# Kernel optimization log

Hardware: AMD Instinct MI355X
Metric: run time of the kernel (lower is better)

The kernel has to match this reference:

```python
import jax, jax.numpy as jnp
import numpy as np

N, DQ, T, H1 = 131072, 256, 4, 512

def setup_inputs() -> dict:
    key = jax.random.key(0)
    k_q, k_w0, k_b0, k_w1, k_z = jax.random.split(key, 5)
    return {
        "q": jax.random.normal(k_q, (N, DQ), dtype=jnp.float32),
        "Z": jax.random.randint(k_z, (N,), 0, T, dtype=jnp.int32),
        "W0": jax.random.normal(k_w0, (T, DQ, H1), dtype=jnp.float32) * (1.0 / np.sqrt(DQ)),
        "b0": jax.random.normal(k_b0, (T, H1), dtype=jnp.float32) * 0.01,
        "W1": jax.random.normal(k_w1, (T, H1), dtype=jnp.float32) * (1.0 / np.sqrt(H1)),
        "b1": jnp.zeros((), dtype=jnp.float32),
    }

def reference(q, Z, W0, b0, W1, b1):
    # Dense grouped-GEMM over all T types (T is small), then select per-atom
    # type result. Avoids materializing the per-atom [N, dq, h1] gathered
    # weight tensor that tf.gather would create.
    h_all = jnp.einsum('nd,tdh->nth', q, W0)              # [N, T, H1]
    h = jnp.take_along_axis(h_all, Z[:, None, None].astype(jnp.int32), axis=1)[:, 0, :]  # [N, H1]
    h = jnp.tanh(h + b0[Z])                               # hidden activations
    F = jnp.einsum('nh,nh->n', h, W1[Z]) + b1             # [N]
    return F
```

## Files before the change

### kernel.cpp

```cpp
#include <hip/hip_runtime.h>
#include <hip/hip_bf16.h>

#define N_ATOMS 131072
#define DQ 256
#define H1 512
#define NTYPES 4
#define TILE_M 64
#define NPAD (N_ATOMS + NTYPES * TILE_M)
#define BLOCKS_PER_TYPE 64

typedef __bf16 bf16x8 __attribute__((ext_vector_type(8)));
typedef float f32x16 __attribute__((ext_vector_type(16)));

__device__ __forceinline__ unsigned short f2bf(float f) {
  unsigned int u = __builtin_bit_cast(unsigned int, f);
  u += 0x7fffu + ((u >> 16) & 1u);
  return (unsigned short)(u >> 16);
}
__device__ __forceinline__ unsigned int pack2(float a, float b) {
  return (unsigned int)f2bf(a) | ((unsigned int)f2bf(b) << 16);
}
__device__ __forceinline__ float fast_tanh(float x) {
  float e = __expf(2.0f * x);
  return 1.0f - 2.0f * __builtin_amdgcn_rcpf(e + 1.0f);
}

__global__ __launch_bounds__(256) void hist_kernel(
    const int* __restrict__ Z, int* __restrict__ perm,
    int* __restrict__ blockcounts)
{
  const int b = blockIdx.x, tid = threadIdx.x;
  const int gid = b * 256 + tid;
  for (int i = gid; i < NPAD; i += 512 * 256) perm[i] = -1;
  __shared__ int lc[NTYPES];
  if (tid < NTYPES) lc[tid] = 0;
  __syncthreads();
  atomicAdd(&lc[Z[gid]], 1);
  __syncthreads();
  if (tid < NTYPES) blockcounts[b * NTYPES + tid] = lc[tid];
}

__global__ __launch_bounds__(256) void w0s_kernel(
    const float* __restrict__ W0, unsigned short* __restrict__ W0s)
{
  __shared__ __align__(16) unsigned short S[64][72];
  const int b = blockIdx.x;
  const int nb = b & 7, kb = (b >> 3) & 3, t = b >> 5;
  const int tid = threadIdx.x;
  const int kl = tid >> 4, nl = (tid & 15) * 4;
#pragma unroll
  for (int r = 0; r < 4; ++r) {
    const int k = r * 16 + kl;
    const float4 v = *(const float4*)&W0[((size_t)(t * DQ + kb * 64 + k)) * H1 + nb * 64 + nl];
    S[nl + 0][k] = f2bf(v.x);
    S[nl + 1][k] = f2bf(v.y);
    S[nl + 2][k] = f2bf(v.z);
    S[nl + 3][k] = f2bf(v.w);
  }
  __syncthreads();
#pragma unroll
  for (int r = 0; r < 2; ++r) {
    const int c = r * 256 + tid;
    const int n = c & 63, kg2l = c >> 6;
    const uint4 v = *(const uint4*)&S[n][kg2l * 8];
    ((uint4*)W0s)[(size_t)(t * 32 + kb * 8 + kg2l) * H1 + nb * 64 + n] = v;
  }
}

__global__ __launch_bounds__(256) void scan_kernel(
    const int* __restrict__ blockcounts, int* __restrict__ padded_off,
    int* __restrict__ cursors)
{
  __shared__ int sums[NTYPES];
  const int tid = threadIdx.x;
  if (tid < NTYPES) sums[tid] = 0;
  __syncthreads();
  const int t = tid & 3;
  int acc = 0;
  for (int b = tid >> 2; b < 512; b += 64) acc += blockcounts[b * 4 + t];
  atomicAdd(&sums[t], acc);
  __syncthreads();
  if (tid == 0) {
    int off = 0;
#pragma unroll
    for (int i = 0; i < NTYPES; ++i) {
      padded_off[i] = off;
      cursors[i] = off;
      off += (sums[i] + TILE_M - 1) & ~(TILE_M - 1);
    }
    padded_off[NTYPES] = off;
  }
}

__global__ __launch_bounds__(256) void scatter_kernel(
    const int* __restrict__ Z, int* __restrict__ cursors, int* __restrict__ perm)
{
  __shared__ int lc[NTYPES], lbase[NTYPES];
  const int tid = threadIdx.x;
  const int gid = blockIdx.x * 256 + tid;
  if (tid < NTYPES) lc[tid] = 0;
  __syncthreads();
  const int t  = Z[gid];
  const int my = atomicAdd(&lc[t], 1);
  __syncthreads();
  if (tid < NTYPES) lbase[tid] = lc[tid] ? atomicAdd(&cursors[tid], lc[tid]) : 0;
  __syncthreads();
  perm[lbase[t] + my] = gid;
}

__device__ __forceinline__ void load_tile(const float* __restrict__ q,
    const int* __restrict__ perm, int row0, int w, int l, float4 ld[8]) {
  int atom = perm[row0 + l];
  if (atom < 0) atom = 0;
  const float* src = q + (size_t)atom * DQ + w * 32;
#pragma unroll
  for (int i = 0; i < 8; ++i) ld[i] = *(const float4*)(src + i * 4);
}

__device__ __forceinline__ void store_tile(unsigned short* Abuf, int w, int l,
                                           const float4 ld[8]) {
#pragma unroll
  for (int i = 0; i < 4; ++i) {
    uint4 v;
    v.x = pack2(ld[2 * i].x, ld[2 * i].y);
    v.y = pack2(ld[2 * i].z, ld[2 * i].w);
    v.z = pack2(ld[2 * i + 1].x, ld[2 * i + 1].y);
    v.w = pack2(ld[2 * i + 1].z, ld[2 * i + 1].w);
    *(uint4*)&Abuf[((w * 4 + i) * 64 + l) * 8] = v;
  }
}

__global__ __launch_bounds__(512, 2) void gemm_kernel(
    const float* __restrict__ q, const int* __restrict__ perm,
    const int* __restrict__ padded_off, const unsigned short* __restrict__ W0s,
    const float* __restrict__ b0, const float* __restrict__ W1,
    const float* __restrict__ b1p, float* __restrict__ out)
{
  __shared__ __align__(16) unsigned short A[2][32 * 64 * 8];
  __shared__ float Fws[8][64];

  const int tid = threadIdx.x;
  const int w = tid >> 6, l = tid & 63;
  const int half = l >> 5, ln = l & 31;

  const int t = blockIdx.x >> 6;
  const int bslot = blockIdx.x & 63;
  const int seg0 = padded_off[t];
  const int ntiles = (padded_off[t + 1] - seg0) >> 6;
  if (bslot >= ntiles) return;

  const int colbase = w * 64;

  float b0v[2], w1v[2];
#pragma unroll
  for (int nt = 0; nt < 2; ++nt) {
    const int c = colbase + nt * 32 + ln;
    b0v[nt] = b0[t * H1 + c];
    w1v[nt] = W1[t * H1 + c];
  }
  const float b1 = b1p[0];

  const unsigned short* Bt = W0s + (size_t)t * (DQ * H1);
  bf16x8 Bf[16][2];
#pragma unroll
  for (int ks = 0; ks < 16; ++ks) {
    const int kg2 = ks * 2 + half;
#pragma unroll
    for (int nt = 0; nt < 2; ++nt)
      Bf[ks][nt] = *(const bf16x8*)(Bt + ((size_t)kg2 * H1 + colbase + nt * 32 + ln) * 8);
  }

  int j = bslot;
  int row0 = seg0 + (j << 6);
  {
    float4 ld[8];
    load_tile(q, perm, row0, w, l, ld);
    store_tile(A[0], w, l, ld);
  }
  __syncthreads();
  int p = 0;

  for (;;) {
    const int jn = j + BLOCKS_PER_TYPE;
    const bool have_next = jn < ntiles;
    const int row0n = seg0 + (jn << 6);

    float4 ld[8];
    if (have_next) load_tile(q, perm, row0n, w, l, ld);

    const unsigned short* Acur = A[p];
    f32x16 acc[2][2];
#pragma unroll
    for (int mt = 0; mt < 2; ++mt)
#pragma unroll
      for (int nt = 0; nt < 2; ++nt) acc[mt][nt] = (f32x16)0.0f;

#pragma unroll
    for (int ks = 0; ks < 16; ++ks) {
      const int kg2 = ks * 2 + half;
      const bf16x8 a0 = *(const bf16x8*)&Acur[(kg2 * 64 + ln) * 8];
      const bf16x8 a1 = *(const bf16x8*)&Acur[(kg2 * 64 + 32 + ln) * 8];
      acc[0][0] = __builtin_amdgcn_mfma_f32_32x32x16_bf16(a0, Bf[ks][0], acc[0][0], 0, 0, 0);
      acc[1][0] = __builtin_amdgcn_mfma_f32_32x32x16_bf16(a1, Bf[ks][0], acc[1][0], 0, 0, 0);
      acc[0][1] = __builtin_amdgcn_mfma_f32_32x32x16_bf16(a0, Bf[ks][1], acc[0][1], 0, 0, 0);
      acc[1][1] = __builtin_amdgcn_mfma_f32_32x32x16_bf16(a1, Bf[ks][1], acc[1][1], 0, 0, 0);
    }

#pragma unroll
    for (int mt = 0; mt < 2; ++mt) {
#pragma unroll
      for (int r = 0; r < 16; ++r) {
        float s = w1v[0] * fast_tanh(acc[mt][0][r] + b0v[0])
                + w1v[1] * fast_tanh(acc[mt][1][r] + b0v[1]);
        s += __shfl_xor(s, 1);
        s += __shfl_xor(s, 2);
        s += __shfl_xor(s, 4);
        s += __shfl_xor(s, 8);
        s += __shfl_xor(s, 16);
        if (ln == 0)
          Fws[w][mt * 32 + (r & 3) + 8 * (r >> 2) + 4 * half] = s;
      }
    }
    __syncthreads();

    if (tid < TILE_M) {
      const int atom = perm[row0 + tid];
      if (atom >= 0) {
        float f = b1;
#pragma unroll
        for (int ww = 0; ww < 8; ++ww) f += Fws[ww][tid];
        out[atom] = f;
      }
    }

    if (!have_next) break;

    store_tile(A[1 - p], w, l, ld);
    __syncthreads();
    p ^= 1;
    j = jn;
    row0 = row0n;
  }
}

extern "C" void kernel_launch(void* const* d_in, const int* in_sizes, int n_in,
                              void* d_out, int out_size, void* d_ws, size_t ws_size,
                              hipStream_t stream) {
  const float* q  = (const float*)d_in[0];
  const int*   Z  = (const int*)d_in[1];
  const float* W0 = (const float*)d_in[2];
  const float* b0 = (const float*)d_in[3];
  const float* W1 = (const float*)d_in[4];
  const float* b1 = (const float*)d_in[5];
  float* out = (float*)d_out;

  char* ws = (char*)d_ws;
  int* blockcounts = (int*)(ws);
  int* padded_off  = (int*)(ws + 8192);
  int* cursors     = (int*)(ws + 8192 + 32);
  int* perm        = (int*)(ws + 8192 + 64);
  unsigned short* W0s = (unsigned short*)(ws + 8192 + 64 + (size_t)NPAD * 4);

  hipLaunchKernelGGL(hist_kernel,    dim3(512), dim3(256), 0, stream, Z, perm, blockcounts);
  hipLaunchKernelGGL(w0s_kernel,     dim3(128), dim3(256), 0, stream, W0, W0s);
  hipLaunchKernelGGL(scan_kernel,    dim3(1),   dim3(256), 0, stream, blockcounts, padded_off, cursors);
  hipLaunchKernelGGL(scatter_kernel, dim3(512), dim3(256), 0, stream, Z, cursors, perm);
  hipLaunchKernelGGL(gemm_kernel,    dim3(NTYPES * BLOCKS_PER_TYPE), dim3(512), 0, stream,
                     q, perm, padded_off, W0s, b0, W1, b1, out);
}
```

Baseline: 320.5 us.

## Fuse prep kernels, coalesce A-tile gather with padded LDS, use DPP reductions

```diff
diff --git a/kernel.cpp b/kernel.cpp
--- a/kernel.cpp
+++ b/kernel.cpp
@@ -8,63 +8,71 @@
 #define TILE_M 64
 #define NPAD (N_ATOMS + NTYPES * TILE_M)
 #define BLOCKS_PER_TYPE 64
+#define ROWPAD 65
 
 typedef __bf16 bf16x8 __attribute__((ext_vector_type(8)));
 typedef float f32x16 __attribute__((ext_vector_type(16)));
 
+__device__ __forceinline__ unsigned int pack2(float a, float b) {
+  unsigned int ua = __builtin_bit_cast(unsigned int, a);
+  unsigned int ub = __builtin_bit_cast(unsigned int, b);
+  ua += 0x7fffu + ((ua >> 16) & 1u);
+  ub += 0x7fffu + ((ub >> 16) & 1u);
+  return __builtin_amdgcn_perm(ub, ua, 0x07060302);
+}
 __device__ __forceinline__ unsigned short f2bf(float f) {
   unsigned int u = __builtin_bit_cast(unsigned int, f);
   u += 0x7fffu + ((u >> 16) & 1u);
   return (unsigned short)(u >> 16);
 }
-__device__ __forceinline__ unsigned int pack2(float a, float b) {
-  return (unsigned int)f2bf(a) | ((unsigned int)f2bf(b) << 16);
-}
 __device__ __forceinline__ float fast_tanh(float x) {
   float e = __expf(2.0f * x);
   return 1.0f - 2.0f * __builtin_amdgcn_rcpf(e + 1.0f);
 }
-
-__global__ __launch_bounds__(256) void hist_kernel(
-    const int* __restrict__ Z, int* __restrict__ perm,
+template <int CTRL>
+__device__ __forceinline__ float dpp_add(float s) {
+  int v = __builtin_amdgcn_mov_dpp(__builtin_bit_cast(int, s), CTRL, 0xF, 0xF, true);
+  return s + __builtin_bit_cast(float, v);
+}
+
+__global__ __launch_bounds__(256) void prep_kernel(
+    const float* __restrict__ W0, const int* __restrict__ Z,
+    unsigned short* __restrict__ W0s, int* __restrict__ perm,
     int* __restrict__ blockcounts)
 {
+  __shared__ int lc[NTYPES];
+  __shared__ __align__(16) unsigned short S[64][72];
   const int b = blockIdx.x, tid = threadIdx.x;
   const int gid = b * 256 + tid;
+
   for (int i = gid; i < NPAD; i += 512 * 256) perm[i] = -1;
-  __shared__ int lc[NTYPES];
   if (tid < NTYPES) lc[tid] = 0;
   __syncthreads();
   atomicAdd(&lc[Z[gid]], 1);
+
+  if (b < 128) {
+    const int nb = b & 7, kb = (b >> 3) & 3, t = b >> 5;
+    const int kl = tid >> 4, nl = (tid & 15) * 4;
+#pragma unroll
+    for (int r = 0; r < 4; ++r) {
+      const int k = r * 16 + kl;
+      const float4 v = *(const float4*)&W0[((size_t)(t * DQ + kb * 64 + k)) * H1 + nb * 64 + nl];
+      S[nl + 0][k] = f2bf(v.x);
+      S[nl + 1][k] = f2bf(v.y);
+      S[nl + 2][k] = f2bf(v.z);
+      S[nl + 3][k] = f2bf(v.w);
+    }
+    __syncthreads();
+#pragma unroll
+    for (int r = 0; r < 2; ++r) {
+      const int c = r * 256 + tid;
+      const int n = c & 63, kg2l = c >> 6;
+      const uint4 v = *(const uint4*)&S[n][kg2l * 8];
+      ((uint4*)W0s)[(size_t)(t * 32 + kb * 8 + kg2l) * H1 + nb * 64 + n] = v;
+    }
+  }
   __syncthreads();
   if (tid < NTYPES) blockcounts[b * NTYPES + tid] = lc[tid];
-}
-
-__global__ __launch_bounds__(256) void w0s_kernel(
-    const float* __restrict__ W0, unsigned short* __restrict__ W0s)
-{
-  __shared__ __align__(16) unsigned short S[64][72];
-  const int b = blockIdx.x;
-  const int nb = b & 7, kb = (b >> 3) & 3, t = b >> 5;
-  const int tid = threadIdx.x;
-  const int kl = tid >> 4, nl = (tid & 15) * 4;
-#pragma unroll
-  for (int r = 0; r < 4; ++r) {
-    const int k = r * 16 + kl;
-    const float4 v = *(const float4*)&W0[((size_t)(t * DQ + kb * 64 + k)) * H1 + nb * 64 + nl];
-    S[nl + 0][k] = f2bf(v.x);
-    S[nl + 1][k] = f2bf(v.y);
-    S[nl + 2][k] = f2bf(v.z);
-    S[nl + 3][k] = f2bf(v.w);
-  }
-  __syncthreads();
-#pragma unroll
-  for (int r = 0; r < 2; ++r) {
-    const int c = r * 256 + tid;
-    const int n = c & 63, kg2l = c >> 6;
-    const uint4 v = *(const uint4*)&S[n][kg2l * 8];
-    ((uint4*)W0s)[(size_t)(t * 32 + kb * 8 + kg2l) * H1 + nb * 64 + n] = v;
-  }
 }
 
 __global__ __launch_bounds__(256) void scan_kernel(
@@ -106,28 +114,6 @@
   if (tid < NTYPES) lbase[tid] = lc[tid] ? atomicAdd(&cursors[tid], lc[tid]) : 0;
   __syncthreads();
   perm[lbase[t] + my] = gid;
-}
-
-__device__ __forceinline__ void load_tile(const float* __restrict__ q,
-    const int* __restrict__ perm, int row0, int w, int l, float4 ld[8]) {
-  int atom = perm[row0 + l];
-  if (atom < 0) atom = 0;
-  const float* src = q + (size_t)atom * DQ + w * 32;
-#pragma unroll
-  for (int i = 0; i < 8; ++i) ld[i] = *(const float4*)(src + i * 4);
-}
-
-__device__ __forceinline__ void store_tile(unsigned short* Abuf, int w, int l,
-                                           const float4 ld[8]) {
-#pragma unroll
-  for (int i = 0; i < 4; ++i) {
-    uint4 v;
-    v.x = pack2(ld[2 * i].x, ld[2 * i].y);
-    v.y = pack2(ld[2 * i].z, ld[2 * i].w);
-    v.z = pack2(ld[2 * i + 1].x, ld[2 * i + 1].y);
-    v.w = pack2(ld[2 * i + 1].z, ld[2 * i + 1].w);
-    *(uint4*)&Abuf[((w * 4 + i) * 64 + l) * 8] = v;
-  }
 }
 
 __global__ __launch_bounds__(512, 2) void gemm_kernel(
@@ -136,7 +122,7 @@
     const float* __restrict__ b0, const float* __restrict__ W1,
     const float* __restrict__ b1p, float* __restrict__ out)
 {
-  __shared__ __align__(16) unsigned short A[2][32 * 64 * 8];
+  __shared__ __align__(16) unsigned short A[2][32 * ROWPAD * 8];
   __shared__ float Fws[8][64];
 
   const int tid = threadIdx.x;
@@ -172,10 +158,15 @@
 
   int j = bslot;
   int row0 = seg0 + (j << 6);
-  {
-    float4 ld[8];
-    load_tile(q, perm, row0, w, l, ld);
-    store_tile(A[0], w, l, ld);
+#pragma unroll
+  for (int i = 0; i < 8; ++i) {
+    int a = perm[row0 + w * 8 + i];
+    if (a < 0) a = 0;
+    const float4 v = *(const float4*)(q + (size_t)a * DQ + l * 4);
+    uint2 u;
+    u.x = pack2(v.x, v.y);
+    u.y = pack2(v.z, v.w);
+    *(uint2*)&A[0][((l >> 1) * ROWPAD + w * 8 + i) * 8 + (l & 1) * 4] = u;
   }
   __syncthreads();
   int p = 0;
@@ -183,10 +174,16 @@
   for (;;) {
     const int jn = j + BLOCKS_PER_TYPE;
     const bool have_next = jn < ntiles;
-    const int row0n = seg0 + (jn << 6);
+    const int rbase = have_next ? seg0 + (jn << 6) : row0;
 
     float4 ld[8];
-    if (have_next) load_tile(q, perm, row0n, w, l, ld);
+#pragma unroll
+    for (int i = 0; i < 8; ++i) {
+      int a = perm[rbase + w * 8 + i];
+      if (a < 0) a = 0;
+      ld[i] = *(const float4*)(q + (size_t)a * DQ + l * 4);
+    }
+    __builtin_amdgcn_sched_barrier(0);
 
     const unsigned short* Acur = A[p];
     f32x16 acc[2][2];
@@ -198,8 +195,8 @@
 #pragma unroll
     for (int ks = 0; ks < 16; ++ks) {
       const int kg2 = ks * 2 + half;
-      const bf16x8 a0 = *(const bf16x8*)&Acur[(kg2 * 64 + ln) * 8];
-      const bf16x8 a1 = *(const bf16x8*)&Acur[(kg2 * 64 + 32 + ln) * 8];
+      const bf16x8 a0 = *(const bf16x8*)&Acur[(kg2 * ROWPAD + ln) * 8];
+      const bf16x8 a1 = *(const bf16x8*)&Acur[(kg2 * ROWPAD + 32 + ln) * 8];
       acc[0][0] = __builtin_amdgcn_mfma_f32_32x32x16_bf16(a0, Bf[ks][0], acc[0][0], 0, 0, 0);
       acc[1][0] = __builtin_amdgcn_mfma_f32_32x32x16_bf16(a1, Bf[ks][0], acc[1][0], 0, 0, 0);
       acc[0][1] = __builtin_amdgcn_mfma_f32_32x32x16_bf16(a0, Bf[ks][1], acc[0][1], 0, 0, 0);
@@ -212,10 +209,10 @@
       for (int r = 0; r < 16; ++r) {
         float s = w1v[0] * fast_tanh(acc[mt][0][r] + b0v[0])
                 + w1v[1] * fast_tanh(acc[mt][1][r] + b0v[1]);
-        s += __shfl_xor(s, 1);
-        s += __shfl_xor(s, 2);
+        s = dpp_add<0xB1>(s);
+        s = dpp_add<0x4E>(s);
         s += __shfl_xor(s, 4);
-        s += __shfl_xor(s, 8);
+        s = dpp_add<0x128>(s);
         s += __shfl_xor(s, 16);
         if (ln == 0)
           Fws[w][mt * 32 + (r & 3) + 8 * (r >> 2) + 4 * half] = s;
@@ -233,13 +230,19 @@
       }
     }
 
+#pragma unroll
+    for (int i = 0; i < 8; ++i) {
+      uint2 u;
+      u.x = pack2(ld[i].x, ld[i].y);
+      u.y = pack2(ld[i].z, ld[i].w);
+      *(uint2*)&A[1 - p][((l >> 1) * ROWPAD + w * 8 + i) * 8 + (l & 1) * 4] = u;
+    }
+
     if (!have_next) break;
-
-    store_tile(A[1 - p], w, l, ld);
     __syncthreads();
     p ^= 1;
     j = jn;
-    row0 = row0n;
+    row0 = rbase;
   }
 }
 
@@ -261,8 +264,7 @@
   int* perm        = (int*)(ws + 8192 + 64);
   unsigned short* W0s = (unsigned short*)(ws + 8192 + 64 + (size_t)NPAD * 4);
 
-  hipLaunchKernelGGL(hist_kernel,    dim3(512), dim3(256), 0, stream, Z, perm, blockcounts);
-  hipLaunchKernelGGL(w0s_kernel,     dim3(128), dim3(256), 0, stream, W0, W0s);
+  hipLaunchKernelGGL(prep_kernel,    dim3(512), dim3(256), 0, stream, W0, Z, W0s, perm, blockcounts);
   hipLaunchKernelGGL(scan_kernel,    dim3(1),   dim3(256), 0, stream, blockcounts, padded_off, cursors);
   hipLaunchKernelGGL(scatter_kernel, dim3(512), dim3(256), 0, stream, Z, cursors, perm);
   hipLaunchKernelGGL(gemm_kernel,    dim3(NTYPES * BLOCKS_PER_TYPE), dim3(512), 0, stream,
```

After: 292.6 us. -8.7%, faster.
